# Kernel tuning notes

Hardware: AMD Instinct MI355X
Metric: run time of the kernel (lower is better)

## Reference

```python
import jax, jax.numpy as jnp
import numpy as np

H = 16           # attn_num
ROPE_THETA = 10000.0

def _rope(x):
    # x: [B, H, S, A]; non-interleaved (rotate-half) RoPE matching RotaryEmb
    A = x.shape[-1]
    S = x.shape[2]
    inv_freq = (1.0 / ROPE_THETA) ** (jnp.arange(0, A, 2, dtype=jnp.float32) / A)  # [A/2]
    t = jnp.arange(S, dtype=jnp.float32)
    freqs = t[:, None] * inv_freq[None, :]            # [S, A/2]
    cos = jnp.cos(freqs)[None, None, :, :]
    sin = jnp.sin(freqs)[None, None, :, :]
    x1, x2 = jnp.split(x, 2, axis=-1)
    y1 = x1 * cos + x2 * sin
    y2 = -x1 * sin + x2 * cos
    return jnp.concatenate([y1, y2], axis=-1).astype(x.dtype)

def setup_inputs() -> dict:
    key = jax.random.key(0)
    kq, kk, kv = jax.random.split(key, 3)
    B, S, D = 2, 2048, 2048
    return {
        "xq": jax.random.normal(kq, (B, S, D), dtype=jnp.float32),
        "xk": jax.random.normal(kk, (B, S, D), dtype=jnp.float32),
        "xv": jax.random.normal(kv, (B, S, D), dtype=jnp.float32),
    }

def reference(xq, xk, xv):
    B, S, D = xq.shape
    A = D // H
    # b s (h a) -> b h s a
    q = xq.reshape(B, S, H, A).transpose(0, 2, 1, 3)
    k = xk.reshape(B, S, H, A).transpose(0, 2, 1, 3)
    v = xv.reshape(B, S, H, A).transpose(0, 2, 1, 3)
    q = _rope(q)
    k = _rope(k)
    scale = 1.0 / jnp.sqrt(jnp.asarray(A, dtype=q.dtype))
    scores = jnp.einsum('bhsa,bhta->bhst', q, k) * scale   # [B,H,S,S]
    causal = jnp.tril(jnp.ones((S, S), dtype=bool))
    scores = jnp.where(causal[None, None, :, :], scores, jnp.asarray(-jnp.inf, scores.dtype))
    probs = jax.nn.softmax(scores, axis=-1)
    out = jnp.einsum('bhst,bhta->bhsa', probs, v)          # [B,H,S,A]
    # b h s a -> b s (h a)
    return out.transpose(0, 2, 1, 3).reshape(B, S, D)
```

## Files before the change

### kernel.cpp

```cpp
#include <hip/hip_runtime.h>
#include <stdint.h>

#define H_HEADS 16
#define ADIM    128
#define SLEN    2048
#define DMODEL  2048

typedef __attribute__((ext_vector_type(8))) short  short8;
typedef __attribute__((ext_vector_type(4))) float  float4v;
typedef __attribute__((ext_vector_type(4))) unsigned short ushort4v;
typedef __attribute__((ext_vector_type(8))) unsigned short ushort8v;

typedef const __attribute__((address_space(1))) unsigned int gas_u32;
typedef __attribute__((address_space(3))) unsigned int las_u32;

union F4 { float4 v; float a[4]; };
union PU { unsigned u[4]; short8 s; };

__device__ __forceinline__ unsigned short f2bf(float f) {
  union { float f; unsigned u; } v; v.f = f;
  unsigned r = v.u + 0x7FFFu + ((v.u >> 16) & 1u);
  return (unsigned short)(r >> 16);
}
__device__ __forceinline__ unsigned cvt_pk_bf16(float lo, float hi) {
  unsigned r;
  asm("v_cvt_pk_bf16_f32 %0, %1, %2" : "=v"(r) : "v"(lo), "v"(hi));
  return r;
}
__device__ __forceinline__ void xswap(unsigned& a, unsigned& b) {
  asm volatile("v_permlane32_swap_b32 %0, %1" : "+v"(a), "+v"(b));
  asm volatile("v_permlane16_swap_b32 %0, %1" : "+v"(a), "+v"(b));
}
__device__ __forceinline__ float fsin01(float r) { float o; asm("v_sin_f32 %0, %1" : "=v"(o) : "v"(r)); return o; }
__device__ __forceinline__ float fcos01(float r) { float o; asm("v_cos_f32 %0, %1" : "=v"(o) : "v"(r)); return o; }
__device__ __forceinline__ float ffract(float x) { float o; asm("v_fract_f32 %0, %1" : "=v"(o) : "v"(x)); return o; }
__device__ __forceinline__ float hexp2(float x)  { float o; asm("v_exp_f32 %0, %1" : "=v"(o) : "v"(x)); return o; }

#define ROPE_C 0.20762050593045935f
#define L2I2PI -2.651496129472319f
#define C2LOG  0.12751879523103988f
#define Z0     8.0f

__global__ __launch_bounds__(256) void prep_k(const float* __restrict__ xk,
                                              unsigned short* __restrict__ kw) {
  int t = blockIdx.x * 256 + threadIdx.x;
  int i4 = t & 15;
  int h  = (t >> 4) & (H_HEADS - 1);
  int s  = (t >> 8) & (SLEN - 1);
  int b  = t >> 19;
  int i0 = i4 * 4;
  long ib = ((long)(b * SLEN + s)) * DMODEL + h * ADIM;
  F4 x1, x2;
  x1.v = *(const float4*)(xk + ib + i0);
  x2.v = *(const float4*)(xk + ib + i0 + 64);
  ushort4v o1, o2;
  #pragma unroll
  for (int j = 0; j < 4; ++j) {
    float rev = (float)s * exp2f(fmaf(-(float)(i0 + j), ROPE_C, L2I2PI));
    float r = ffract(rev);
    float sn = fsin01(r), cs = fcos01(r);
    o1[j] = f2bf( x1.a[j] * cs + x2.a[j] * sn);
    o2[j] = f2bf(-x1.a[j] * sn + x2.a[j] * cs);
  }
  long row = ((long)((b * H_HEADS + h) * SLEN + s)) * ADIM;
  int swz = s & 7;
  int c1 = ((((i0     ) >> 3) ^ swz) << 3) | (i0 & 7);
  int c2 = ((((i0 + 64) >> 3) ^ swz) << 3) | (i0 & 7);
  *(ushort4v*)(kw + row + c1) = o1;
  *(ushort4v*)(kw + row + c2) = o2;
}

__global__ __launch_bounds__(256) void prep_v(const float* __restrict__ xv,
                                              unsigned short* __restrict__ vw) {
  __shared__ float lv[16 * 129];
  int jt = blockIdx.x;
  int bh = blockIdx.y;
  int b = bh >> 4, h = bh & (H_HEADS - 1);
  int t = threadIdx.x;
  #pragma unroll
  for (int it = 0; it < 2; ++it) {
    int id  = it * 256 + t;
    int row = id >> 5;
    int c4  = (id & 31) * 4;
    F4 x;
    x.v = *(const float4*)(xv + ((long)(b * SLEN + jt * 16 + row)) * DMODEL + h * ADIM + c4);
    #pragma unroll
    for (int jj = 0; jj < 4; ++jj) lv[row * 129 + c4 + jj] = x.a[jj];
  }
  __syncthreads();
  int d = t >> 1, half = t & 1;
  ushort8v o;
  #pragma unroll
  for (int jj = 0; jj < 8; ++jj) o[jj] = f2bf(lv[(half * 8 + jj) * 129 + d]);
  *(ushort8v*)(vw + ((long)(bh * 128 + jt)) * 2048 + d * 16 + half * 8) = o;
}

__global__ __launch_bounds__(256, 3) void attn_fwd(const float* __restrict__ xq,
                                                   const unsigned short* __restrict__ kw,
                                                   const unsigned short* __restrict__ vw,
                                                   float* __restrict__ out) {
  __shared__ __align__(16) unsigned char sbuf[36864];
  unsigned short* kB = (unsigned short*)sbuf;
  unsigned short* vB = (unsigned short*)(sbuf + 16384);
  float4v* mergeO = (float4v*)sbuf;
  float4v* mergeL = (float4v*)(sbuf + 32768);

  int n = blockIdx.x;
  int xcd = n & 7, j = n >> 3;
  int bh = xcd * 4 + (j & 3);
  int c  = 31 - (j >> 2);
  int b = bh >> 4, h = bh & (H_HEADS - 1);
  int t = threadIdx.x, l = t & 63, w = t >> 6;
  int wq = w >> 1, g = w & 1;
  int lq = l & 15, gq = l >> 4, lq7 = lq & 7;
  int basew = c * 64 + wq * 32;
  int sq0 = basew + lq, sq1 = basew + 16 + lq;

  short8 qf0[4], qf1[4];
  auto ROPEQ = [&](int sq, short8 (&qf)[4]) {
    const float* qsrc = xq + ((long)(b * SLEN + sq)) * DMODEL + h * ADIM;
    float q32[4][8];
    #pragma unroll
    for (int cc = 0; cc < 4; ++cc) {
      F4 lo, hi;
      lo.v = *(const float4*)(qsrc + cc * 32 + gq * 8);
      hi.v = *(const float4*)(qsrc + cc * 32 + gq * 8 + 4);
      #pragma unroll
      for (int jj = 0; jj < 4; ++jj) { q32[cc][jj] = lo.a[jj]; q32[cc][jj + 4] = hi.a[jj]; }
    }
    #pragma unroll
    for (int cc = 0; cc < 2; ++cc) {
      #pragma unroll
      for (int jj = 0; jj < 8; ++jj) {
        int a = cc * 32 + gq * 8 + jj;
        float rev = (float)sq * exp2f(fmaf(-(float)a, ROPE_C, L2I2PI));
        float r = ffract(rev);
        float sn = fsin01(r), cs = fcos01(r);
        qf[cc    ][jj] = (short)f2bf( q32[cc][jj] * cs + q32[cc + 2][jj] * sn);
        qf[cc + 2][jj] = (short)f2bf(-q32[cc][jj] * sn + q32[cc + 2][jj] * cs);
      }
    }
  };
  ROPEQ(sq0, qf0);
  ROPEQ(sq1, qf1);

  float4v acc0[8], acc1[8], lacc0, lacc1;
  #pragma unroll
  for (int i = 0; i < 8; ++i) { acc0[i] = (float4v){0.f,0.f,0.f,0.f}; acc1[i] = (float4v){0.f,0.f,0.f,0.f}; }
  lacc0 = (float4v){0.f,0.f,0.f,0.f};
  lacc1 = (float4v){0.f,0.f,0.f,0.f};
  const float4v Z4 = (float4v){0.f,0.f,0.f,0.f};

  PU ones;
  ones.u[0] = 0x3F803F80u; ones.u[1] = 0x3F803F80u; ones.u[2] = 0x3F803F80u; ones.u[3] = 0x3F803F80u;

  const unsigned short* kbase = kw + (long)bh * SLEN * ADIM;
  const unsigned short* vbase = vw + (long)bh * 128 * 2048;

  unsigned short* kst[2] = { kB + (g * 2 + 0) * 2048, kB + (g * 2 + 1) * 2048 };
  unsigned short* vst[2] = { vB + (g * 2 + 0) * 2048, vB + (g * 2 + 1) * 2048 };
  const unsigned short* klr[2] = { kst[0] + lq * 128, kst[1] + lq * 128 };
  const unsigned short* vlr[2] = { vst[0] + lq * 16 + (gq & 1) * 8,
                                   vst[1] + lq * 16 + (gq & 1) * 8 };
  int koff[4];
  #pragma unroll
  for (int cc = 0; cc < 4; ++cc) koff[cc] = ((cc * 4 + gq) ^ lq7) << 3;

  auto STAGE = [&](unsigned short* kd, unsigned short* vd, int tile) {
    const unsigned short* ks = kbase + (long)tile * 2048;
    const unsigned short* vs = vbase + (long)tile * 2048;
    #pragma unroll
    for (int i = 0; i < 2; ++i) {
      int seg = wq * 2 + i;
      __builtin_amdgcn_global_load_lds((gas_u32*)(ks + seg * 512 + l * 8),
                                       (las_u32*)&kd[seg * 512], 16, 0, 0);
      __builtin_amdgcn_global_load_lds((gas_u32*)(vs + seg * 512 + l * 8),
                                       (las_u32*)&vd[seg * 512], 16, 0, 0);
    }
  };

  auto SMAX = [&](float4v sv, int sq, bool dg, int tj, float4v& lac) -> short8 {
    float p[4];
    #pragma unroll
    for (int r = 0; r < 4; ++r) {
      float e = fmaf(sv[r], C2LOG, -Z0);
      if (dg && (tj * 16 + gq * 4 + r > sq)) e = -1e30f;
      p[r] = hexp2(e);
    }
    unsigned L0 = cvt_pk_bf16(p[0], p[1]);
    unsigned H0 = cvt_pk_bf16(p[2], p[3]);
    unsigned L1 = 0u, H1 = 0u;
    xswap(L0, L1);
    xswap(H0, H1);
    PU a;
    a.u[0] = L0; a.u[1] = H0; a.u[2] = L1; a.u[3] = H1;
    lac = __builtin_amdgcn_mfma_f32_16x16x32_bf16(a.s, ones.s, lac, 0, 0, 0);
    return a.s;
  };

  int M = 2 * c + 2;

  auto ITER = [&](int m, const unsigned short* klrow, const unsigned short* vlrow,
                  unsigned short* kn, unsigned short* vn) {
    if (m + 1 < M) STAGE(kn, vn, 2 * (m + 1) + g);
    int tj = 2 * m + g;

    float4v s0, s1;
    __builtin_amdgcn_s_setprio(1);
    {
      short8 kf = *(const short8*)&klrow[koff[0]];
      s0 = __builtin_amdgcn_mfma_f32_16x16x32_bf16(kf, qf0[0], Z4, 0, 0, 0);
      s1 = __builtin_amdgcn_mfma_f32_16x16x32_bf16(kf, qf1[0], Z4, 0, 0, 0);
      #pragma unroll
      for (int cc = 1; cc < 4; ++cc) {
        kf = *(const short8*)&klrow[koff[cc]];
        s0 = __builtin_amdgcn_mfma_f32_16x16x32_bf16(kf, qf0[cc], s0, 0, 0, 0);
        s1 = __builtin_amdgcn_mfma_f32_16x16x32_bf16(kf, qf1[cc], s1, 0, 0, 0);
      }
    }
    __builtin_amdgcn_s_setprio(0);

    bool dg = (tj * 16 + 15 > basew);
    short8 pa0 = SMAX(s0, sq0, dg, tj, lacc0);
    short8 pa1 = SMAX(s1, sq1, dg, tj, lacc1);

    __builtin_amdgcn_s_setprio(1);
    #pragma unroll
    for (int db = 0; db < 8; ++db) {
      short8 vb = *(const short8*)&vlrow[db * 256];
      acc0[db] = __builtin_amdgcn_mfma_f32_16x16x32_bf16(pa0, vb, acc0[db], 0, 0, 0);
      acc1[db] = __builtin_amdgcn_mfma_f32_16x16x32_bf16(pa1, vb, acc1[db], 0, 0, 0);
    }
    __builtin_amdgcn_s_setprio(0);

    asm volatile("s_waitcnt vmcnt(0)" ::: "memory");
    __builtin_amdgcn_s_barrier();
  };

  STAGE(kst[0], vst[0], g);
  asm volatile("s_waitcnt vmcnt(0)" ::: "memory");
  __builtin_amdgcn_s_barrier();

  for (int m = 0; m < M; m += 2) {
    ITER(m,     klr[0], vlr[0], kst[1], vst[1]);
    ITER(m + 1, klr[1], vlr[1], kst[0], vst[0]);
  }

  if (g == 1) {
    float4v* dst = mergeO + wq * 1024;
    #pragma unroll
    for (int i = 0; i < 8; ++i) {
      dst[i * 64 + l]       = acc0[i];
      dst[(8 + i) * 64 + l] = acc1[i];
    }
    float4v* ld = mergeL + wq * 128;
    ld[l]      = lacc0;
    ld[64 + l] = lacc1;
  }
  __builtin_amdgcn_s_barrier();

  if (g == 0) {
    const float4v* src = mergeO + wq * 1024;
    #pragma unroll
    for (int i = 0; i < 8; ++i) {
      float4v b0 = src[i * 64 + l];
      float4v b1 = src[(8 + i) * 64 + l];
      #pragma unroll
      for (int r = 0; r < 4; ++r) { acc0[i][r] += b0[r]; acc1[i][r] += b1[r]; }
    }
    const float4v* ls = mergeL + wq * 128;
    float4v lb0 = ls[l], lb1 = ls[64 + l];
    #pragma unroll
    for (int r = 0; r < 4; ++r) { lacc0[r] += lb0[r]; lacc1[r] += lb1[r]; }

    auto EPI = [&](int base, float4v& lac, float4v (&acc)[8]) {
      float linv[4];
      #pragma unroll
      for (int r = 0; r < 4; ++r) linv[r] = 1.0f / lac[r];
      #pragma unroll
      for (int db = 0; db < 8; ++db)
        #pragma unroll
        for (int r = 0; r < 4; ++r)
          out[((long)(b * SLEN + base + gq * 4 + r)) * DMODEL + h * ADIM + db * 16 + lq]
            = acc[db][r] * linv[r];
    };
    EPI(basew,      lacc0, acc0);
    EPI(basew + 16, lacc1, acc1);
  }
}

extern "C" void kernel_launch(void* const* d_in, const int* in_sizes, int n_in,
                              void* d_out, int out_size, void* d_ws, size_t ws_size,
                              hipStream_t stream) {
  const float* xq = (const float*)d_in[0];
  const float* xk = (const float*)d_in[1];
  const float* xv = (const float*)d_in[2];
  float* outp = (float*)d_out;
  int B = in_sizes[0] / (SLEN * DMODEL);
  size_t perT = (size_t)B * H_HEADS * SLEN * ADIM;
  unsigned short* kw = (unsigned short*)d_ws;
  unsigned short* vw = kw + perT;

  prep_k<<<dim3(B * 2048), 256, 0, stream>>>(xk, kw);
  prep_v<<<dim3(128, B * H_HEADS), 256, 0, stream>>>(xv, vw);
  attn_fwd<<<dim3(B * H_HEADS * 32), 256, 0, stream>>>(xq, kw, vw, outp);
}
```

Baseline: 81.83 us.

## Use 32-key tiles with full-K PV MFMA and load V directly from global

Each warp group now processes 32-key tiles instead of 16, so the softmax output fills the full 32-wide K dimension of the PV MFMA instead of zero-padding half of it. That halves the PV MFMA count per key. V is re-laid out by prep_v into 32-row tiles and read directly from global/L2 into registers rather than staged through LDS, which frees LDS for larger K tiles. A trailing odd iteration and an activity guard handle causal tiles past the diagonal. The risks are global-load latency on the V reads and extra wasted work on partially masked tiles.

```diff
diff --git a/kernel.cpp b/kernel.cpp
--- a/kernel.cpp
+++ b/kernel.cpp
@@ -9,7 +9,6 @@
 typedef __attribute__((ext_vector_type(8))) short  short8;
 typedef __attribute__((ext_vector_type(4))) float  float4v;
 typedef __attribute__((ext_vector_type(4))) unsigned short ushort4v;
-typedef __attribute__((ext_vector_type(8))) unsigned short ushort8v;
 
 typedef const __attribute__((address_space(1))) unsigned int gas_u32;
 typedef __attribute__((address_space(3))) unsigned int las_u32;
@@ -72,27 +71,33 @@
 
 __global__ __launch_bounds__(256) void prep_v(const float* __restrict__ xv,
                                               unsigned short* __restrict__ vw) {
-  __shared__ float lv[16 * 129];
+  __shared__ float lv[32 * 129];
   int jt = blockIdx.x;
   int bh = blockIdx.y;
   int b = bh >> 4, h = bh & (H_HEADS - 1);
   int t = threadIdx.x;
   #pragma unroll
-  for (int it = 0; it < 2; ++it) {
+  for (int it = 0; it < 4; ++it) {
     int id  = it * 256 + t;
     int row = id >> 5;
     int c4  = (id & 31) * 4;
     F4 x;
-    x.v = *(const float4*)(xv + ((long)(b * SLEN + jt * 16 + row)) * DMODEL + h * ADIM + c4);
+    x.v = *(const float4*)(xv + ((long)(b * SLEN + jt * 32 + row)) * DMODEL + h * ADIM + c4);
     #pragma unroll
     for (int jj = 0; jj < 4; ++jj) lv[row * 129 + c4 + jj] = x.a[jj];
   }
   __syncthreads();
-  int d = t >> 1, half = t & 1;
-  ushort8v o;
-  #pragma unroll
-  for (int jj = 0; jj < 8; ++jj) o[jj] = f2bf(lv[(half * 8 + jj) * 129 + d]);
-  *(ushort8v*)(vw + ((long)(bh * 128 + jt)) * 2048 + d * 16 + half * 8) = o;
+  unsigned short* vt = vw + ((long)(bh * 64 + jt)) * 4096;
+  #pragma unroll
+  for (int it = 0; it < 4; ++it) {
+    int id = it * 256 + t;
+    int d  = id >> 3;
+    int i  = id & 7;
+    ushort4v o;
+    #pragma unroll
+    for (int jj = 0; jj < 4; ++jj) o[jj] = f2bf(lv[(4 * i + jj) * 129 + d]);
+    *(ushort4v*)(vt + d * 32 + i * 4) = o;
+  }
 }
 
 __global__ __launch_bounds__(256, 3) void attn_fwd(const float* __restrict__ xq,
@@ -101,7 +106,6 @@
                                                    float* __restrict__ out) {
   __shared__ __align__(16) unsigned char sbuf[36864];
   unsigned short* kB = (unsigned short*)sbuf;
-  unsigned short* vB = (unsigned short*)(sbuf + 16384);
   float4v* mergeO = (float4v*)sbuf;
   float4v* mergeL = (float4v*)(sbuf + 32768);
 
@@ -155,41 +159,40 @@
   ones.u[0] = 0x3F803F80u; ones.u[1] = 0x3F803F80u; ones.u[2] = 0x3F803F80u; ones.u[3] = 0x3F803F80u;
 
   const unsigned short* kbase = kw + (long)bh * SLEN * ADIM;
-  const unsigned short* vbase = vw + (long)bh * 128 * 2048;
-
-  unsigned short* kst[2] = { kB + (g * 2 + 0) * 2048, kB + (g * 2 + 1) * 2048 };
-  unsigned short* vst[2] = { vB + (g * 2 + 0) * 2048, vB + (g * 2 + 1) * 2048 };
+  const unsigned short* vbase = vw + (long)bh * 64 * 4096;
+
+  unsigned short* kst[2] = { kB + (g * 2 + 0) * 4096, kB + (g * 2 + 1) * 4096 };
   const unsigned short* klr[2] = { kst[0] + lq * 128, kst[1] + lq * 128 };
-  const unsigned short* vlr[2] = { vst[0] + lq * 16 + (gq & 1) * 8,
-                                   vst[1] + lq * 16 + (gq & 1) * 8 };
   int koff[4];
   #pragma unroll
   for (int cc = 0; cc < 4; ++cc) koff[cc] = ((cc * 4 + gq) ^ lq7) << 3;
-
-  auto STAGE = [&](unsigned short* kd, unsigned short* vd, int tile) {
-    const unsigned short* ks = kbase + (long)tile * 2048;
-    const unsigned short* vs = vbase + (long)tile * 2048;
-    #pragma unroll
-    for (int i = 0; i < 2; ++i) {
-      int seg = wq * 2 + i;
+  int vlane = lq * 32 + gq * 8;
+
+  auto STAGE = [&](unsigned short* kd, int tile) {
+    const unsigned short* ks = kbase + (long)tile * 4096;
+    #pragma unroll
+    for (int i = 0; i < 4; ++i) {
+      int seg = wq * 4 + i;
       __builtin_amdgcn_global_load_lds((gas_u32*)(ks + seg * 512 + l * 8),
                                        (las_u32*)&kd[seg * 512], 16, 0, 0);
-      __builtin_amdgcn_global_load_lds((gas_u32*)(vs + seg * 512 + l * 8),
-                                       (las_u32*)&vd[seg * 512], 16, 0, 0);
     }
   };
 
-  auto SMAX = [&](float4v sv, int sq, bool dg, int tj, float4v& lac) -> short8 {
-    float p[4];
-    #pragma unroll
-    for (int r = 0; r < 4; ++r) {
-      float e = fmaf(sv[r], C2LOG, -Z0);
-      if (dg && (tj * 16 + gq * 4 + r > sq)) e = -1e30f;
-      p[r] = hexp2(e);
+  auto SMAX = [&](float4v (&sv)[2], int sq, bool dg, int tj, float4v& lac) -> short8 {
+    float p[8];
+    #pragma unroll
+    for (int kb = 0; kb < 2; ++kb) {
+      #pragma unroll
+      for (int r = 0; r < 4; ++r) {
+        float e = fmaf(sv[kb][r], C2LOG, -Z0);
+        if (dg && (tj * 32 + kb * 16 + gq * 4 + r > sq)) e = -1e30f;
+        p[kb * 4 + r] = hexp2(e);
+      }
     }
     unsigned L0 = cvt_pk_bf16(p[0], p[1]);
     unsigned H0 = cvt_pk_bf16(p[2], p[3]);
-    unsigned L1 = 0u, H1 = 0u;
+    unsigned L1 = cvt_pk_bf16(p[4], p[5]);
+    unsigned H1 = cvt_pk_bf16(p[6], p[7]);
     xswap(L0, L1);
     xswap(H0, H1);
     PU a;
@@ -198,53 +201,76 @@
     return a.s;
   };
 
-  int M = 2 * c + 2;
-
-  auto ITER = [&](int m, const unsigned short* klrow, const unsigned short* vlrow,
-                  unsigned short* kn, unsigned short* vn) {
-    if (m + 1 < M) STAGE(kn, vn, 2 * (m + 1) + g);
+  int M = c + 1;
+
+  auto ITER = [&](int m, const unsigned short* klrow, unsigned short* kn) {
+    if (m + 1 < M) STAGE(kn, 2 * (m + 1) + g);
     int tj = 2 * m + g;
-
-    float4v s0, s1;
-    __builtin_amdgcn_s_setprio(1);
-    {
-      short8 kf = *(const short8*)&klrow[koff[0]];
-      s0 = __builtin_amdgcn_mfma_f32_16x16x32_bf16(kf, qf0[0], Z4, 0, 0, 0);
-      s1 = __builtin_amdgcn_mfma_f32_16x16x32_bf16(kf, qf1[0], Z4, 0, 0, 0);
-      #pragma unroll
-      for (int cc = 1; cc < 4; ++cc) {
-        kf = *(const short8*)&klrow[koff[cc]];
-        s0 = __builtin_amdgcn_mfma_f32_16x16x32_bf16(kf, qf0[cc], s0, 0, 0, 0);
-        s1 = __builtin_amdgcn_mfma_f32_16x16x32_bf16(kf, qf1[cc], s1, 0, 0, 0);
-      }
-    }
-    __builtin_amdgcn_s_setprio(0);
-
-    bool dg = (tj * 16 + 15 > basew);
-    short8 pa0 = SMAX(s0, sq0, dg, tj, lacc0);
-    short8 pa1 = SMAX(s1, sq1, dg, tj, lacc1);
-
-    __builtin_amdgcn_s_setprio(1);
-    #pragma unroll
-    for (int db = 0; db < 8; ++db) {
-      short8 vb = *(const short8*)&vlrow[db * 256];
-      acc0[db] = __builtin_amdgcn_mfma_f32_16x16x32_bf16(pa0, vb, acc0[db], 0, 0, 0);
-      acc1[db] = __builtin_amdgcn_mfma_f32_16x16x32_bf16(pa1, vb, acc1[db], 0, 0, 0);
-    }
-    __builtin_amdgcn_s_setprio(0);
-
+    bool act = (tj * 32 <= basew + 31);
+    if (act) {
+      const unsigned short* vt = vbase + (long)tj * 4096;
+      short8 vbA[4];
+      #pragma unroll
+      for (int db = 0; db < 4; ++db)
+        vbA[db] = *(const short8*)(vt + db * 512 + vlane);
+
+      float4v s0[2], s1[2];
+      __builtin_amdgcn_s_setprio(1);
+      {
+        #pragma unroll
+        for (int kb = 0; kb < 2; ++kb) {
+          short8 kf = *(const short8*)&klrow[kb * 2048 + koff[0]];
+          s0[kb] = __builtin_amdgcn_mfma_f32_16x16x32_bf16(kf, qf0[0], Z4, 0, 0, 0);
+          s1[kb] = __builtin_amdgcn_mfma_f32_16x16x32_bf16(kf, qf1[0], Z4, 0, 0, 0);
+        }
+        #pragma unroll
+        for (int cc = 1; cc < 4; ++cc) {
+          #pragma unroll
+          for (int kb = 0; kb < 2; ++kb) {
+            short8 kf = *(const short8*)&klrow[kb * 2048 + koff[cc]];
+            s0[kb] = __builtin_amdgcn_mfma_f32_16x16x32_bf16(kf, qf0[cc], s0[kb], 0, 0, 0);
+            s1[kb] = __builtin_amdgcn_mfma_f32_16x16x32_bf16(kf, qf1[cc], s1[kb], 0, 0, 0);
+          }
+        }
+      }
+      __builtin_amdgcn_s_setprio(0);
+
+      bool dg = (tj * 32 + 31 > basew);
+      short8 pa0 = SMAX(s0, sq0, dg, tj, lacc0);
+      short8 pa1 = SMAX(s1, sq1, dg, tj, lacc1);
+
+      short8 vbB[4];
+      #pragma unroll
+      for (int db = 0; db < 4; ++db)
+        vbB[db] = *(const short8*)(vt + (db + 4) * 512 + vlane);
+
+      __builtin_amdgcn_s_setprio(1);
+      #pragma unroll
+      for (int db = 0; db < 4; ++db) {
+        acc0[db] = __builtin_amdgcn_mfma_f32_16x16x32_bf16(pa0, vbA[db], acc0[db], 0, 0, 0);
+        acc1[db] = __builtin_amdgcn_mfma_f32_16x16x32_bf16(pa1, vbA[db], acc1[db], 0, 0, 0);
+      }
+      #pragma unroll
+      for (int db = 0; db < 4; ++db) {
+        acc0[db + 4] = __builtin_amdgcn_mfma_f32_16x16x32_bf16(pa0, vbB[db], acc0[db + 4], 0, 0, 0);
+        acc1[db + 4] = __builtin_amdgcn_mfma_f32_16x16x32_bf16(pa1, vbB[db], acc1[db + 4], 0, 0, 0);
+      }
+      __builtin_amdgcn_s_setprio(0);
+    }
     asm volatile("s_waitcnt vmcnt(0)" ::: "memory");
     __builtin_amdgcn_s_barrier();
   };
 
-  STAGE(kst[0], vst[0], g);
+  STAGE(kst[0], g);
   asm volatile("s_waitcnt vmcnt(0)" ::: "memory");
   __builtin_amdgcn_s_barrier();
 
-  for (int m = 0; m < M; m += 2) {
-    ITER(m,     klr[0], vlr[0], kst[1], vst[1]);
-    ITER(m + 1, klr[1], vlr[1], kst[0], vst[0]);
-  }
+  int m = 0;
+  for (; m + 2 <= M; m += 2) {
+    ITER(m,     klr[0], kst[1]);
+    ITER(m + 1, klr[1], kst[0]);
+  }
+  if (m < M) ITER(m, klr[0], kst[1]);
 
   if (g == 1) {
     float4v* dst = mergeO + wq * 1024;
@@ -302,6 +328,6 @@
   unsigned short* vw = kw + perT;
 
   prep_k<<<dim3(B * 2048), 256, 0, stream>>>(xk, kw);
-  prep_v<<<dim3(128, B * H_HEADS), 256, 0, stream>>>(xv, vw);
+  prep_v<<<dim3(64, B * H_HEADS), 256, 0, stream>>>(xv, vw);
   attn_fwd<<<dim3(B * H_HEADS * 32), 256, 0, stream>>>(xq, kw, vw, outp);
 }
```

Result: slower. 90.35 us (+10.4%).
